# Optimization experiments

Measured on AMD Instinct MI355X. Metric: run time of the kernel, lower is better.

Reference implementation:

```python
import jax, jax.numpy as jnp
import numpy as np

N_EMB = 512
EMB_DIM = 64
DECAY = 0.99
EPS = 1e-5


def setup_inputs() -> dict:
    key = jax.random.key(0)
    k1, k2 = jax.random.split(key)
    x = jax.random.normal(k1, (32, EMB_DIM, 64, 64), dtype=jnp.float32)
    weight = jax.random.uniform(k2, (EMB_DIM, N_EMB), dtype=jnp.float32)  # rd_init=True: torch.rand(emb_dim, n_emb)
    cluster_size = jnp.zeros((N_EMB,), dtype=jnp.float32)
    embed_avg = weight  # buffer initialized as embed.clone()
    return {"x": x, "weight": weight, "cluster_size": cluster_size, "embed_avg": embed_avg}


def reference(x, weight, cluster_size, embed_avg):
    B, D, H, W = x.shape
    n_emb = weight.shape[1]
    # (B, D, H, W) -> (N, D) tokens
    flat = jnp.transpose(x, (0, 2, 3, 1)).reshape(-1, D)
    dist = (jnp.sum(flat * flat, axis=1, keepdims=True)
            - 2.0 * (flat @ weight)
            + jnp.sum(weight * weight, axis=0)[None, :])
    argmin = jnp.argmin(dist, axis=1)                      # (N,)
    quant = jnp.take(weight.T, argmin, axis=0)             # gather -> (N, D)
    result = jnp.transpose(quant.reshape(B, H, W, D), (0, 3, 1, 2))  # (B, D, H, W)

    # --- EMA codebook update (training branch) ---
    ones = jnp.ones(argmin.shape, dtype=x.dtype)
    n_idx = jax.ops.segment_sum(ones, argmin, num_segments=n_emb)    # onehot.sum(0)
    n_idx = jnp.where(n_idx == 0, jnp.ones_like(n_idx), n_idx)       # clamp empty clusters to 1
    new_cluster_size = DECAY * cluster_size + (1.0 - DECAY) * n_idx
    embed_sum = jax.ops.segment_sum(flat, argmin, num_segments=n_emb).T  # flatten.T @ onehot -> (D, n_emb)
    new_embed_avg = DECAY * embed_avg + (1.0 - DECAY) * embed_sum
    n = jnp.sum(new_cluster_size)
    cs = (new_cluster_size + EPS) / (n + n_emb * EPS) * n
    new_weight = new_embed_avg / cs[None, :]

    return result, argmin.reshape(B, H, W), new_weight, new_cluster_size, new_embed_avg
```

## Files before the change

kernel.cpp:

```cpp
#include <hip/hip_runtime.h>

#define NEMB 512
#define EMB 64
#define BSTR 262144
#define DECAYF 0.99f
#define OMDF 0.01f
#define EPSF 1e-5f
#define GAP_T 0.006f
#define QCAP 32768

typedef __attribute__((ext_vector_type(8))) short bf16x8;
typedef __attribute__((ext_vector_type(4))) float f32x4;

__device__ __forceinline__ unsigned short f2bf(float f) {
    unsigned u = __float_as_uint(f);
    return (unsigned short)((u + 0x7FFFu + ((u >> 16) & 1u)) >> 16);
}
__device__ __forceinline__ float bf2f(unsigned short h) {
    return __uint_as_float(((unsigned)h) << 16);
}

__device__ __forceinline__ void gl2lds16(const void* g, void* l) {
    __builtin_amdgcn_global_load_lds(
        (const __attribute__((address_space(1))) unsigned int*)g,
        (__attribute__((address_space(3))) unsigned int*)l, 16, 0, 0);
}

__global__ void prep_kernel(const float* __restrict__ w,
                            unsigned short* __restrict__ wh, unsigned short* __restrict__ wl,
                            float* __restrict__ wsq,
                            float* __restrict__ cnt_ws, unsigned* __restrict__ gcnt) {
    int j = threadIdx.x;
    if (blockIdx.x < 8) {
        int d0 = blockIdx.x << 3;
        bf16x8 hb, lb;
#pragma unroll
        for (int i = 0; i < 8; ++i) {
            float v = w[(d0 + i) * NEMB + j];
            unsigned short h = f2bf(v);
            hb[i] = (short)h;
            lb[i] = (short)f2bf(v - bf2f(h));
        }
        *(bf16x8*)(wh + j * EMB + d0) = hb;
        *(bf16x8*)(wl + j * EMB + d0) = lb;
    } else {
        float s = 0.f;
#pragma unroll
        for (int d = 0; d < EMB; ++d) { float v = w[d * NEMB + j]; s = fmaf(v, v, s); }
        wsq[j] = s;
        cnt_ws[j] = 0.f;
        if (j == 0) *gcnt = 0u;
    }
}

#define UPD(S1, J1, S2, J2, s_, j_) do { \
    if (s_ < S1 || (s_ == S1 && j_ < J1)) { S2 = S1; J2 = J1; S1 = s_; J1 = j_; } \
    else if (s_ < S2 || (s_ == S2 && j_ < J2)) { S2 = s_; J2 = j_; } } while (0)

__global__ __launch_bounds__(512, 4) void vq_main(
    const float* __restrict__ x,
    const unsigned short* __restrict__ wh, const unsigned short* __restrict__ wl,
    const float* __restrict__ wsq,
    float* __restrict__ out_arg, unsigned* __restrict__ gcnt, int* __restrict__ queue)
{
    __shared__ __align__(16) unsigned char ubuf[65536];
    __shared__ float wsq_s[NEMB];

    float* xt = (float*)ubuf;
    unsigned short* whs = (unsigned short*)ubuf;
    unsigned short* wls = whs + 16384;

    const int tid = threadIdx.x;
    const int blk = blockIdx.x;
    const int b    = blk >> 4;
    const int hgrp = blk & 15;
    const int t0 = b * 4096 + hgrp * 256;
    const float* xbase = x + b * BSTR + hgrp * 256;

    const int lane = tid & 63;
    const int wave = tid >> 6;

#pragma unroll
    for (int it = 0; it < 8; ++it) {
        int d = wave + (it << 3);
        gl2lds16(xbase + d * 4096 + (lane << 2), xt + d * 256);
    }
    wsq_s[tid] = wsq[tid];
    __syncthreads();

    const int l15  = lane & 15;
    const int quad = lane >> 4;
    const int wbase = wave << 5;

    bf16x8 ah[2][2], al[2][2];
    float xq[2][4];
#pragma unroll
    for (int mt = 0; mt < 2; ++mt) {
        int m = wbase + (mt << 4) + l15;
        float sq = 0.f;
#pragma unroll
        for (int ks = 0; ks < 2; ++ks) {
            int k0 = (ks << 5) + (quad << 3);
            bf16x8 hh, ll;
#pragma unroll
            for (int i = 0; i < 8; ++i) {
                float v = xt[(k0 + i) * 256 + m];
                sq = fmaf(v, v, sq);
                unsigned short h = f2bf(v);
                hh[i] = (short)h;
                ll[i] = (short)f2bf(v - bf2f(h));
            }
            ah[mt][ks] = hh; al[mt][ks] = ll;
        }
        sq += __shfl_xor(sq, 16, 64);
        sq += __shfl_xor(sq, 32, 64);
#pragma unroll
        for (int r = 0; r < 4; ++r)
            xq[mt][r] = __shfl(sq, (quad << 2) + r, 64);
    }
    __syncthreads();

    float v1[2][4], v2[2][4];
    int   j1[2][4];
#pragma unroll
    for (int mt = 0; mt < 2; ++mt)
#pragma unroll
        for (int r = 0; r < 4; ++r) { v1[mt][r] = 3.4e38f; v2[mt][r] = 3.4e38f; j1[mt][r] = 0; }

    const int m7 = l15 & 7;
    const int s0off = ((quad ^ m7) << 3);
    const int s1off = (((4 | quad) ^ m7) << 3);

    for (int half = 0; half < 2; ++half) {
#pragma unroll
        for (int it = 0; it < 8; ++it) {
            int g0  = (wave << 6) + (it << 9);
            int arr = g0 >> 11;
            int win0 = g0 & 2047;
            int win = win0 + lane;
            int row = win >> 3, slot = win & 7;
            const unsigned short* src =
                (arr ? wl : wh) + ((half << 8) + row) * EMB + ((slot ^ (row & 7)) << 3);
            unsigned short* ldst = (arr ? wls : whs) + (win0 << 3);
            gl2lds16(src, ldst);
        }
        __syncthreads();

        const int nbase = half << 8;
#pragma unroll 2
        for (int it = 0; it < 16; ++it) {
            const int ib = ((it << 4) + l15) << 6;
            bf16x8 b0 = *(const bf16x8*)(whs + ib + s0off);
            bf16x8 b1 = *(const bf16x8*)(whs + ib + s1off);
            bf16x8 b2 = *(const bf16x8*)(wls + ib + s0off);
            bf16x8 b3 = *(const bf16x8*)(wls + ib + s1off);
            const int n = nbase + (it << 4) + l15;
            float wq = wsq_s[n];

            f32x4 acc0 = (f32x4){0.f, 0.f, 0.f, 0.f};
            f32x4 acc1 = (f32x4){0.f, 0.f, 0.f, 0.f};
            acc0 = __builtin_amdgcn_mfma_f32_16x16x32_bf16(ah[0][0], b0, acc0, 0, 0, 0);
            acc1 = __builtin_amdgcn_mfma_f32_16x16x32_bf16(ah[1][0], b0, acc1, 0, 0, 0);
            acc0 = __builtin_amdgcn_mfma_f32_16x16x32_bf16(ah[0][1], b1, acc0, 0, 0, 0);
            acc1 = __builtin_amdgcn_mfma_f32_16x16x32_bf16(ah[1][1], b1, acc1, 0, 0, 0);
            acc0 = __builtin_amdgcn_mfma_f32_16x16x32_bf16(ah[0][0], b2, acc0, 0, 0, 0);
            acc1 = __builtin_amdgcn_mfma_f32_16x16x32_bf16(ah[1][0], b2, acc1, 0, 0, 0);
            acc0 = __builtin_amdgcn_mfma_f32_16x16x32_bf16(ah[0][1], b3, acc0, 0, 0, 0);
            acc1 = __builtin_amdgcn_mfma_f32_16x16x32_bf16(ah[1][1], b3, acc1, 0, 0, 0);
            acc0 = __builtin_amdgcn_mfma_f32_16x16x32_bf16(al[0][0], b0, acc0, 0, 0, 0);
            acc1 = __builtin_amdgcn_mfma_f32_16x16x32_bf16(al[1][0], b0, acc1, 0, 0, 0);
            acc0 = __builtin_amdgcn_mfma_f32_16x16x32_bf16(al[0][1], b1, acc0, 0, 0, 0);
            acc1 = __builtin_amdgcn_mfma_f32_16x16x32_bf16(al[1][1], b1, acc1, 0, 0, 0);

#pragma unroll
            for (int r = 0; r < 4; ++r) {
                float s0 = fmaf(-2.f, acc0[r], xq[0][r] + wq);
                bool p0 = s0 < v1[0][r];
                float mx0 = fmaxf(s0, v1[0][r]);
                v1[0][r] = fminf(s0, v1[0][r]);
                v2[0][r] = fminf(v2[0][r], mx0);
                j1[0][r] = p0 ? n : j1[0][r];

                float s1 = fmaf(-2.f, acc1[r], xq[1][r] + wq);
                bool p1 = s1 < v1[1][r];
                float mx1 = fmaxf(s1, v1[1][r]);
                v1[1][r] = fminf(s1, v1[1][r]);
                v2[1][r] = fminf(v2[1][r], mx1);
                j1[1][r] = p1 ? n : j1[1][r];
            }
        }
        __syncthreads();
    }

#pragma unroll
    for (int mt = 0; mt < 2; ++mt)
#pragma unroll
        for (int r = 0; r < 4; ++r) {
            float a1 = v1[mt][r], a2 = v2[mt][r];
            int   aj = j1[mt][r];
#pragma unroll
            for (int msk = 1; msk < 16; msk <<= 1) {
                float o1 = __shfl_xor(a1, msk, 64);
                int   oj = __shfl_xor(aj, msk, 64);
                float o2 = __shfl_xor(a2, msk, 64);
                bool take = (o1 < a1) || (o1 == a1 && oj < aj);
                float mx = fmaxf(a1, o1);
                a2 = fminf(fminf(a2, o2), mx);
                a1 = fminf(a1, o1);
                aj = take ? oj : aj;
            }
            v1[mt][r] = a1; v2[mt][r] = a2; j1[mt][r] = aj;
        }

    if (l15 == 0) {
#pragma unroll
        for (int mt = 0; mt < 2; ++mt)
#pragma unroll
            for (int r = 0; r < 4; ++r) {
                int gt = t0 + wbase + (mt << 4) + (quad << 2) + r;
                out_arg[gt] = (float)j1[mt][r];
                if (v2[mt][r] - v1[mt][r] < GAP_T) {
                    unsigned idx = atomicAdd(gcnt, 1u);
                    if (idx < QCAP) queue[idx] = gt;
                }
            }
    }
}

__global__ __launch_bounds__(256) void refine_kernel(
    const float* __restrict__ x, const float* __restrict__ w,
    const float* __restrict__ wsq, const unsigned* __restrict__ gcnt,
    const int* __restrict__ queue, float* __restrict__ out_arg)
{
    __shared__ float wsq_s[NEMB];
    const int tid = threadIdx.x;
    wsq_s[tid] = wsq[tid];
    wsq_s[tid + 256] = wsq[tid + 256];
    __syncthreads();

    unsigned nfu = *gcnt;
    const int nf = (int)(nfu < (unsigned)QCAP ? nfu : (unsigned)QCAP);
    const int lane = tid & 63;
    const int gw = (blockIdx.x << 2) + (tid >> 6);

    for (int i = gw; i < nf; i += 1024) {
        const int t = queue[i] & 131071;
        const int b = t >> 12, pos = t & 4095;
        float xd = x[b * BSTR + lane * 4096 + pos];
        float xqv = xd * xd;
#pragma unroll
        for (int mk = 1; mk < 64; mk <<= 1) xqv += __shfl_xor(xqv, mk, 64);

        float accv[8];
#pragma unroll
        for (int k = 0; k < 8; ++k) accv[k] = 0.f;
#pragma unroll 4
        for (int d = 0; d < EMB; ++d) {
            float4 wa = *(const float4*)(w + d * NEMB + (lane << 2));
            float4 wb = *(const float4*)(w + d * NEMB + 256 + (lane << 2));
            float xv = __shfl(xd, d, 64);
            accv[0] = fmaf(xv, wa.x, accv[0]);
            accv[1] = fmaf(xv, wa.y, accv[1]);
            accv[2] = fmaf(xv, wa.z, accv[2]);
            accv[3] = fmaf(xv, wa.w, accv[3]);
            accv[4] = fmaf(xv, wb.x, accv[4]);
            accv[5] = fmaf(xv, wb.y, accv[5]);
            accv[6] = fmaf(xv, wb.z, accv[6]);
            accv[7] = fmaf(xv, wb.w, accv[7]);
        }

        float S1 = 3.4e38f, S2 = 3.4e38f; int J1 = 0, J2 = 0;
#pragma unroll
        for (int k = 0; k < 8; ++k) {
            int j = (k < 4) ? ((lane << 2) + k) : (256 + (lane << 2) + k - 4);
            float s = (xqv - 2.f * accv[k]) + wsq_s[j];
            UPD(S1, J1, S2, J2, s, j);
        }
#pragma unroll
        for (int mk = 1; mk < 64; mk <<= 1) {
            float os1 = __shfl_xor(S1, mk, 64); int oj1 = __shfl_xor(J1, mk, 64);
            float os2 = __shfl_xor(S2, mk, 64); int oj2 = __shfl_xor(J2, mk, 64);
            UPD(S1, J1, S2, J2, os1, oj1);
            UPD(S1, J1, S2, J2, os2, oj2);
        }

        int jm = J1;
        if (S2 - S1 < 1e-3f) {
            float w1 = w[lane * NEMB + J1];
            float w2 = w[lane * NEMB + J2];
            double e1 = (double)w1 * (double)w1 - 2.0 * (double)xd * (double)w1;
            double e2 = (double)w2 * (double)w2 - 2.0 * (double)xd * (double)w2;
#pragma unroll
            for (int mk = 1; mk < 64; mk <<= 1) {
                e1 += __shfl_xor(e1, mk, 64);
                e2 += __shfl_xor(e2, mk, 64);
            }
            if (e2 < e1 || (e2 == e1 && J2 < J1)) jm = J2;
        }
        if (lane == 0) out_arg[t] = (float)jm;
    }
}

__global__ __launch_bounds__(512, 4) void es_kernel(
    const float* __restrict__ x, const float* __restrict__ arg,
    float* __restrict__ es_p, float* __restrict__ cnt_ws)
{
    __shared__ unsigned short xh[16384];
    __shared__ int args_s[256];
    __shared__ float cacc[NEMB];

    const int tid = threadIdx.x;
    const int blk = blockIdx.x;
    const int flavor = blk & 1;
    const int chunk  = blk >> 1;
    const int b = chunk >> 3;
    const int tpos0 = (chunk & 7) << 9;

    cacc[tid] = 0.f;

    const int lane = tid & 63;
    const int wave = tid >> 6;
    const int l15  = lane & 15;
    const int quad = lane >> 4;
    const int jb   = wave << 5;

    f32x4 acc[4][2];
#pragma unroll
    for (int m = 0; m < 4; ++m)
#pragma unroll
        for (int nc = 0; nc < 2; ++nc) acc[m][nc] = (f32x4){0.f, 0.f, 0.f, 0.f};

    for (int st = 0; st < 2; ++st) {
        const int tpos = tpos0 + (st << 8);
#pragma unroll
        for (int it = 0; it < 8; ++it) {
            int idx = tid + (it << 9);
            int d = idx >> 6, q = idx & 63;
            float4 g = *(const float4*)(x + b * BSTR + d * 4096 + tpos + (q << 2));
            int c = q >> 1, half = q & 1;
            int off = d * 256 + ((c ^ (d & 7)) << 3) + (half << 2);
            ushort4 hv = {f2bf(g.x), f2bf(g.y), f2bf(g.z), f2bf(g.w)};
            *(ushort4*)(xh + off) = hv;
        }
        if (tid < 256) args_s[tid] = ((int)arg[b * 4096 + tpos + tid]) & 511;
        __syncthreads();

        if (flavor == 0 && tid < 256) atomicAdd(&cacc[args_s[tid]], 1.f);

#pragma unroll
        for (int kk = 0; kk < 8; ++kk) {
            bf16x8 a_[4];
#pragma unroll
            for (int m = 0; m < 4; ++m) {
                int d = (m << 4) + l15;
                int coff = ((((kk << 2) + quad) ^ (d & 7)) << 3);
                a_[m] = *(const bf16x8*)(xh + d * 256 + coff);
            }
            int argv[8];
            const int kb = (kk << 5) + (quad << 3);
#pragma unroll
            for (int i = 0; i < 8; ++i) argv[i] = args_s[kb + i];
#pragma unroll
            for (int nc = 0; nc < 2; ++nc) {
                const int jg = (flavor << 8) + jb + (nc << 4) + l15;
                bf16x8 bf;
#pragma unroll
                for (int i = 0; i < 8; ++i) bf[i] = (argv[i] == jg) ? (short)0x3F80 : (short)0;
#pragma unroll
                for (int m = 0; m < 4; ++m)
                    acc[m][nc] = __builtin_amdgcn_mfma_f32_16x16x32_bf16(a_[m], bf, acc[m][nc], 0, 0, 0);
            }
        }
        __syncthreads();
    }

    float* ep = es_p + blk * 16384;
#pragma unroll
    for (int m = 0; m < 4; ++m)
#pragma unroll
        for (int nc = 0; nc < 2; ++nc) {
            const int jl = jb + (nc << 4) + l15;
#pragma unroll
            for (int r = 0; r < 4; ++r) {
                const int d = (m << 4) + (quad << 2) + r;
                ep[d * 256 + jl] = acc[m][nc][r];
            }
        }
    if (flavor == 0) {
        float v = cacc[tid];
        if (v != 0.f) atomicAdd(&cnt_ws[tid], v);
    }
}

__global__ __launch_bounds__(256) void finalize_kernel(
    const float* __restrict__ cs_in, const float* __restrict__ avg_in,
    const float* __restrict__ cnt_ws, const float* __restrict__ es_p,
    float* __restrict__ out_w, float* __restrict__ out_ncs,
    float* __restrict__ out_avg) {
    __shared__ float red[256];
    const int tid = threadIdx.x;
    const int d  = blockIdx.x >> 1;
    const int jh = blockIdx.x & 1;

    float c0 = cnt_ws[tid], c1 = cnt_ws[tid + 256];
    float ncs0 = DECAYF * cs_in[tid] + OMDF * ((c0 == 0.f) ? 1.f : c0);
    float ncs1 = DECAYF * cs_in[tid + 256] + OMDF * ((c1 == 0.f) ? 1.f : c1);
    red[tid] = ncs0 + ncs1;
    __syncthreads();
    for (int s = 128; s > 0; s >>= 1) {
        if (tid < s) red[tid] += red[tid + s];
        __syncthreads();
    }
    const float n = red[0];

    const float* ep = es_p + jh * 16384 + d * 256 + tid;
    float s = 0.f;
#pragma unroll 16
    for (int c = 0; c < 256; ++c) s += ep[c * 32768];

    const float ncs = jh ? ncs1 : ncs0;
    const float csj = (ncs + EPSF) / (n + (float)NEMB * EPSF) * n;
    const int o = d * NEMB + (jh << 8) + tid;
    const float navg = DECAYF * avg_in[o] + OMDF * s;
    out_avg[o] = navg;
    out_w[o] = navg / csj;
    if (blockIdx.x == 0) { out_ncs[tid] = ncs0; out_ncs[tid + 256] = ncs1; }
}

__global__ __launch_bounds__(512) void result_kernel(
    const float* __restrict__ w, const float* __restrict__ arg,
    float* __restrict__ out_result)
{
    __shared__ float wrow8[8 * 512];
    const int tid = threadIdx.x;
    const int grp = blockIdx.x >> 6;
    const int chunk = blockIdx.x & 63;
#pragma unroll
    for (int d = 0; d < 8; ++d)
        wrow8[(d << 9) + tid] = w[((grp << 3) + d) * NEMB + tid];
    __syncthreads();

    const int t = (chunk << 11) + (tid << 2);
    const int o = (t >> 12) * BSTR + (t & 4095);
    float4 a4 = *(const float4*)(arg + t);
    int j0 = ((int)a4.x) & 511, j1 = ((int)a4.y) & 511;
    int j2 = ((int)a4.z) & 511, j3 = ((int)a4.w) & 511;
#pragma unroll
    for (int d = 0; d < 8; ++d) {
        const int dg = (grp << 3) + d;
        float4 r4 = {wrow8[(d << 9) + j0], wrow8[(d << 9) + j1],
                     wrow8[(d << 9) + j2], wrow8[(d << 9) + j3]};
        *(float4*)(out_result + o + dg * 4096) = r4;
    }
}

extern "C" void kernel_launch(void* const* d_in, const int* in_sizes, int n_in,
                              void* d_out, int out_size, void* d_ws, size_t ws_size,
                              hipStream_t stream) {
    (void)in_sizes; (void)n_in; (void)out_size; (void)ws_size;
    const float* x   = (const float*)d_in[0];
    const float* w   = (const float*)d_in[1];
    const float* cs  = (const float*)d_in[2];
    const float* avg = (const float*)d_in[3];

    float* out = (float*)d_out;
    float* out_result = out;
    float* out_arg    = out + 8388608;
    float* out_w      = out + 8519680;
    float* out_ncs    = out + 8552448;
    float* out_avg    = out + 8552960;
    float* es_p       = out;

    char* wsb = (char*)d_ws;
    unsigned short* wh = (unsigned short*)wsb;
    unsigned short* wl = (unsigned short*)(wsb + 65536);
    float* wsq      = (float*)(wsb + 131072);
    float* cnt_ws   = (float*)(wsb + 133120);
    unsigned* gcnt  = (unsigned*)(wsb + 135168);
    int* queue      = (int*)(wsb + 135232);

    prep_kernel<<<9, 512, 0, stream>>>(w, wh, wl, wsq, cnt_ws, gcnt);
    vq_main<<<512, 512, 0, stream>>>(x, wh, wl, wsq, out_arg, gcnt, queue);
    refine_kernel<<<256, 256, 0, stream>>>(x, w, wsq, gcnt, queue, out_arg);
    es_kernel<<<512, 512, 0, stream>>>(x, out_arg, es_p, cnt_ws);
    finalize_kernel<<<128, 256, 0, stream>>>(cs, avg, cnt_ws, es_p, out_w, out_ncs, out_avg);
    result_kernel<<<512, 512, 0, stream>>>(w, out_arg, out_result);
}
```

Measured before the change: 181.4 us.

## Halve LDS buffer by staging x and codebook in smaller chunks

```diff
diff --git a/kernel.cpp b/kernel.cpp
--- a/kernel.cpp
+++ b/kernel.cpp
@@ -63,12 +63,12 @@
     const float* __restrict__ wsq,
     float* __restrict__ out_arg, unsigned* __restrict__ gcnt, int* __restrict__ queue)
 {
-    __shared__ __align__(16) unsigned char ubuf[65536];
+    __shared__ __align__(16) unsigned char ubuf[32768];
     __shared__ float wsq_s[NEMB];
 
-    float* xt = (float*)ubuf;
-    unsigned short* whs = (unsigned short*)ubuf;
-    unsigned short* wls = whs + 16384;
+    float* xhf = (float*)ubuf;
+    unsigned short* whq = (unsigned short*)ubuf;
+    unsigned short* wlq = whq + 8192;
 
     const int tid = threadIdx.x;
     const int blk = blockIdx.x;
@@ -79,39 +79,61 @@
 
     const int lane = tid & 63;
     const int wave = tid >> 6;
-
-#pragma unroll
-    for (int it = 0; it < 8; ++it) {
-        int d = wave + (it << 3);
-        gl2lds16(xbase + d * 4096 + (lane << 2), xt + d * 256);
-    }
-    wsq_s[tid] = wsq[tid];
-    __syncthreads();
-
     const int l15  = lane & 15;
     const int quad = lane >> 4;
     const int wbase = wave << 5;
 
+#pragma unroll
+    for (int it = 0; it < 4; ++it) {
+        int d = wave + (it << 3);
+        gl2lds16(xbase + d * 4096 + (lane << 2), xhf + d * 256);
+    }
+    wsq_s[tid] = wsq[tid];
+    __syncthreads();
+
     bf16x8 ah[2][2], al[2][2];
-    float xq[2][4];
+    float sqa[2] = {0.f, 0.f};
+
 #pragma unroll
     for (int mt = 0; mt < 2; ++mt) {
         int m = wbase + (mt << 4) + l15;
-        float sq = 0.f;
-#pragma unroll
-        for (int ks = 0; ks < 2; ++ks) {
-            int k0 = (ks << 5) + (quad << 3);
-            bf16x8 hh, ll;
-#pragma unroll
-            for (int i = 0; i < 8; ++i) {
-                float v = xt[(k0 + i) * 256 + m];
-                sq = fmaf(v, v, sq);
-                unsigned short h = f2bf(v);
-                hh[i] = (short)h;
-                ll[i] = (short)f2bf(v - bf2f(h));
-            }
-            ah[mt][ks] = hh; al[mt][ks] = ll;
-        }
+        int k0l = quad << 3;
+        bf16x8 hh, ll;
+#pragma unroll
+        for (int i = 0; i < 8; ++i) {
+            float v = xhf[(k0l + i) * 256 + m];
+            sqa[mt] = fmaf(v, v, sqa[mt]);
+            unsigned short h = f2bf(v);
+            hh[i] = (short)h;
+            ll[i] = (short)f2bf(v - bf2f(h));
+        }
+        ah[mt][0] = hh; al[mt][0] = ll;
+    }
+    __syncthreads();
+
+#pragma unroll
+    for (int it = 0; it < 4; ++it) {
+        int d = wave + (it << 3);
+        gl2lds16(xbase + (32 + d) * 4096 + (lane << 2), xhf + d * 256);
+    }
+    __syncthreads();
+
+    float xq[2][4];
+#pragma unroll
+    for (int mt = 0; mt < 2; ++mt) {
+        int m = wbase + (mt << 4) + l15;
+        int k0l = quad << 3;
+        bf16x8 hh, ll;
+#pragma unroll
+        for (int i = 0; i < 8; ++i) {
+            float v = xhf[(k0l + i) * 256 + m];
+            sqa[mt] = fmaf(v, v, sqa[mt]);
+            unsigned short h = f2bf(v);
+            hh[i] = (short)h;
+            ll[i] = (short)f2bf(v - bf2f(h));
+        }
+        ah[mt][1] = hh; al[mt][1] = ll;
+        float sq = sqa[mt];
         sq += __shfl_xor(sq, 16, 64);
         sq += __shfl_xor(sq, 32, 64);
 #pragma unroll
@@ -131,29 +153,28 @@
     const int s0off = ((quad ^ m7) << 3);
     const int s1off = (((4 | quad) ^ m7) << 3);
 
-    for (int half = 0; half < 2; ++half) {
-#pragma unroll
+#pragma unroll
+    for (int it = 0; it < 4; ++it) {
+        int g0 = (wave << 6) + (it << 9);
+        int arr = g0 >> 10;
+        int win0 = g0 & 1023;
+        int win = win0 + lane;
+        int row = win >> 3, slot = win & 7;
+        const unsigned short* src =
+            (arr ? wl : wh) + row * EMB + ((slot ^ (row & 7)) << 3);
+        gl2lds16(src, (arr ? wlq : whq) + (win0 << 3));
+    }
+    __syncthreads();
+
+    for (int q = 0; q < 4; ++q) {
+        const int nbase = q << 7;
+#pragma unroll 2
         for (int it = 0; it < 8; ++it) {
-            int g0  = (wave << 6) + (it << 9);
-            int arr = g0 >> 11;
-            int win0 = g0 & 2047;
-            int win = win0 + lane;
-            int row = win >> 3, slot = win & 7;
-            const unsigned short* src =
-                (arr ? wl : wh) + ((half << 8) + row) * EMB + ((slot ^ (row & 7)) << 3);
-            unsigned short* ldst = (arr ? wls : whs) + (win0 << 3);
-            gl2lds16(src, ldst);
-        }
-        __syncthreads();
-
-        const int nbase = half << 8;
-#pragma unroll 2
-        for (int it = 0; it < 16; ++it) {
             const int ib = ((it << 4) + l15) << 6;
-            bf16x8 b0 = *(const bf16x8*)(whs + ib + s0off);
-            bf16x8 b1 = *(const bf16x8*)(whs + ib + s1off);
-            bf16x8 b2 = *(const bf16x8*)(wls + ib + s0off);
-            bf16x8 b3 = *(const bf16x8*)(wls + ib + s1off);
+            bf16x8 b0 = *(const bf16x8*)(whq + ib + s0off);
+            bf16x8 b1 = *(const bf16x8*)(whq + ib + s1off);
+            bf16x8 b2 = *(const bf16x8*)(wlq + ib + s0off);
+            bf16x8 b3 = *(const bf16x8*)(wlq + ib + s1off);
             const int n = nbase + (it << 4) + l15;
             float wq = wsq_s[n];
 
@@ -190,6 +211,20 @@
             }
         }
         __syncthreads();
+        if (q < 3) {
+#pragma unroll
+            for (int it = 0; it < 4; ++it) {
+                int g0 = (wave << 6) + (it << 9);
+                int arr = g0 >> 10;
+                int win0 = g0 & 1023;
+                int win = win0 + lane;
+                int row = win >> 3, slot = win & 7;
+                const unsigned short* src =
+                    (arr ? wl : wh) + (((q + 1) << 7) + row) * EMB + ((slot ^ (row & 7)) << 3);
+                gl2lds16(src, (arr ? wlq : whq) + (win0 << 3));
+            }
+            __syncthreads();
+        }
     }
 
 #pragma unroll
```

After: 175.6 us. -3.2%, faster.
